# Kernel optimization log

Hardware: AMD Instinct MI355X
Metric: run time of the kernel (lower is better)

## Reference

```python
import jax, jax.numpy as jnp
import numpy as np

B, C, H = 256, 5, 13
N_AGENTS = 8192
N_EDGES = 262144
ACT = 21


def setup_inputs() -> dict:
    key = jax.random.key(0)
    ks = jax.random.split(key, 20)
    inp = {
        "x": jax.random.normal(ks[0], (B, C, H, H), jnp.float32),
        "x_msg": jax.random.normal(ks[1], (N_AGENTS,), jnp.float32),
        "edge_index": jax.random.randint(ks[2], (N_EDGES, 2), 0, N_AGENTS, jnp.int64 if jax.config.jax_enable_x64 else jnp.int32),
        "action": jax.random.randint(ks[3], (B,), 0, ACT, jnp.int32),
        # params (orthogonal init approximated by scaled normal; math identical)
        "conv1_w": jax.random.normal(ks[4], (32, 5, 3, 3), jnp.float32) * 0.1,
        "conv1_b": jnp.zeros((32,), jnp.float32),
        "conv2_w": jax.random.normal(ks[5], (64, 32, 3, 3), jnp.float32) * 0.05,
        "conv2_b": jnp.zeros((64,), jnp.float32),
        "fc_w": jax.random.normal(ks[6], (512, 1024), jnp.float32) * 0.03,
        "fc_b": jnp.zeros((512,), jnp.float32),
        "fc_mu_w": jax.random.normal(ks[7], (ACT, 512), jnp.float32) * 0.01,
        "fc_mu_b": jnp.zeros((ACT,), jnp.float32),
        "msg_w": jax.random.normal(ks[8], (N_AGENTS, 512), jnp.float32) * 0.01,
        "msg_b": jnp.zeros((N_AGENTS,), jnp.float32),
        "gcn1_w": jax.random.normal(ks[9], (2, 16), jnp.float32) * 0.5,
        "gcn1_b": jnp.zeros((16,), jnp.float32),
        "gcn2_w": jax.random.normal(ks[10], (16, N_AGENTS), jnp.float32) * 0.1,
        "gcn2_b": jnp.zeros((N_AGENTS,), jnp.float32),
    }
    return inp


def _gcn_norm(edge_index, n):
    # add self-loops; edge_index is (E,2) [src, dst]
    loops = jnp.arange(n, dtype=edge_index.dtype)
    src = jnp.concatenate([edge_index[:, 0], loops])
    dst = jnp.concatenate([edge_index[:, 1], loops])
    deg = jax.ops.segment_sum(jnp.ones_like(src, jnp.float32), dst, num_segments=n)
    dinv = jnp.where(deg > 0, jax.lax.rsqrt(deg), 0.0)
    norm = dinv[src] * dinv[dst]  # [E+n]
    return src, dst, norm


def _gcn_conv(h, src, dst, norm, W, b, n):
    hw = h @ W  # [n, out]
    out = jax.ops.segment_sum(norm[:, None] * hw[src], dst, num_segments=n)
    return out + b


def reference(x, x_msg, edge_index, action, conv1_w, conv1_b, conv2_w, conv2_b,
              fc_w, fc_b, fc_mu_w, fc_mu_b, msg_w, msg_b,
              gcn1_w, gcn1_b, gcn2_w, gcn2_b):
    dn = ("NCHW", "OIHW", "NCHW")
    h = jax.lax.conv_general_dilated(x, conv1_w, (2, 2), "VALID", dimension_numbers=dn)
    h = jax.nn.relu(h + conv1_b[None, :, None, None])  # [B,32,6,6]
    h = jax.lax.conv_general_dilated(h, conv2_w, (1, 1), "VALID", dimension_numbers=dn)
    h = jax.nn.relu(h + conv2_b[None, :, None, None])  # [B,64,4,4]
    h = h.reshape(h.shape[0], -1)  # [B,1024], torch NCHW flatten order
    hidden = jax.nn.relu(h @ fc_w.T + fc_b)  # [B,512]

    logits = hidden @ fc_mu_w.T + fc_mu_b            # [B,21]
    actor_encoding = hidden @ msg_w.T + msg_b        # [B,N]

    # Categorical log_prob / entropy for the given action
    logp = jax.nn.log_softmax(logits, axis=-1)
    log_prob = jnp.take_along_axis(logp, action[:, None], axis=1)[:, 0]
    entropy = -jnp.sum(jnp.exp(logp) * logp, axis=-1)

    # GNN message branch (eval mode: dropout is identity)
    feats = jnp.stack([x_msg, actor_encoding[0]], axis=0).T  # [N,2]
    n = feats.shape[0]
    src, dst, norm = _gcn_norm(edge_index, n)
    g = jax.nn.relu(_gcn_conv(feats, src, dst, norm, gcn1_w, gcn1_b, n))  # [N,16]
    g = _gcn_conv(g, src, dst, norm, gcn2_w, gcn2_b, n)                    # [N,N]
    msg_out = jax.nn.log_softmax(g, axis=1).mean(axis=1)                   # [N]

    return (action, msg_out, log_prob, entropy)
```

## Files before the change

kernel.cpp:

```cpp
#include <hip/hip_runtime.h>
#include <hip/hip_bf16.h>

#define NB 256
#define NACT 21
#define NA 8192
#define NE 262144
#define CSR_CAP 128
#define LOG2E 1.44269504f

#if __has_builtin(__builtin_amdgcn_exp2f)
#define EXP2F(x) __builtin_amdgcn_exp2f(x)
#else
#define EXP2F(x) exp2f(x)
#endif

typedef __attribute__((ext_vector_type(8))) short short8;
typedef __attribute__((ext_vector_type(4))) float float4v;

__device__ inline float wsum64(float v) {
#pragma unroll
  for (int m = 32; m > 0; m >>= 1) v += __shfl_xor(v, m, 64);
  return v;
}

__device__ inline unsigned short f2bf(float f) {
  union { __hip_bfloat16 h; unsigned short u; } cv;
  cv.h = __float2bfloat16(f);
  return cv.u;
}

__global__ void k_init(const int* action, int* cnt, float* out) {
  int i = blockIdx.x * 256 + threadIdx.x;
  if (i < NA) cnt[i] = 0;
  if (i < NB) out[i] = (float)action[i];
}

__global__ __launch_bounds__(512, 4) void k_prep(
    const int* __restrict__ edges, const float* __restrict__ fcw,
    const float* __restrict__ g2w, const float* __restrict__ g2b,
    unsigned short* fcwbf, unsigned short* w2t, float* wpart, int* cnt, int* csr) {
  __shared__ float red[16][17];
  __shared__ float b2s[16];
  int t = threadIdx.x, blk = blockIdx.x;
  {
    int e = blk * 512 + t;
    int s = edges[2 * e], d = edges[2 * e + 1];
    int slot = atomicAdd(&cnt[d], 1);
    if (slot < CSR_CAP) csr[d * CSR_CAP + slot] = s;
  }
  {
    int base = (blk * 512 + t) * 2;
    float2 v = *(const float2*)&fcw[base];
    fcwbf[base + 0] = f2bf(v.x);
    fcwbf[base + 1] = f2bf(v.y);
  }
  {
    if (t < 256) {
      int jj = t >> 4, k = t & 15;
      int j = blk * 16 + jj;
      float w = g2w[k * 8192 + j];
      w2t[j * 16 + k] = f2bf(w);
      red[jj][k] = w;
    }
    if (t < 16) b2s[t] = g2b[blk * 16 + t];
    __syncthreads();
    if (t < 16) {
      float s = 0.0f;
#pragma unroll
      for (int q = 0; q < 16; q++) s += red[q][t];
      wpart[blk * 17 + t] = s;
    } else if (t == 16) {
      float s = 0.0f;
#pragma unroll
      for (int q = 0; q < 16; q++) s += b2s[q];
      wpart[blk * 17 + 16] = s;
    }
  }
}

__global__ __launch_bounds__(512, 2) void k_conv(
    const float* __restrict__ x, const float* __restrict__ c1w, const float* __restrict__ c1b,
    const float* __restrict__ c2w, const float* __restrict__ c2b, unsigned short* h1024bf) {
  __shared__ float xs[845];
  __shared__ float w1s[1440];
  __shared__ float c1s[1152];
  __shared__ float w2s[64 * 73];
  int t = threadIdx.x, blk = blockIdx.x;
  for (int i = t; i < 845; i += 512) xs[i] = x[blk * 845 + i];
  for (int i = t; i < 1440; i += 512) w1s[i] = c1w[i];
  __syncthreads();
  for (int idx = t; idx < 1152; idx += 512) {
    int oc = idx / 36, p = idx - oc * 36;
    int oy = p / 6, ox = p - oy * 6;
    float acc = c1b[oc];
    const float* wp = &w1s[oc * 45];
#pragma unroll
    for (int ic = 0; ic < 5; ic++)
#pragma unroll
      for (int ky = 0; ky < 3; ky++)
#pragma unroll
        for (int kx = 0; kx < 3; kx++)
          acc += xs[ic * 169 + (oy * 2 + ky) * 13 + ox * 2 + kx] * wp[ic * 9 + ky * 3 + kx];
    c1s[idx] = fmaxf(acc, 0.0f);
  }
  int p = t & 15, oc2 = t >> 4;
  int oy = p >> 2, ox = p & 3;
  float a0 = c2b[oc2 * 2 + 0], a1 = c2b[oc2 * 2 + 1];
  for (int icb = 0; icb < 32; icb += 8) {
    __syncthreads();
    for (int i = t; i < 4608; i += 512) {
      int oc = i / 72, r = i - oc * 72;
      w2s[oc * 73 + r] = c2w[oc * 288 + icb * 9 + r];
    }
    __syncthreads();
#pragma unroll
    for (int ic = 0; ic < 8; ic++) {
#pragma unroll
      for (int ky = 0; ky < 3; ky++) {
#pragma unroll
        for (int kx = 0; kx < 3; kx++) {
          float cvv = c1s[(icb + ic) * 36 + (oy + ky) * 6 + ox + kx];
          int wi = ic * 9 + ky * 3 + kx;
          a0 += cvv * w2s[(oc2 * 2 + 0) * 73 + wi];
          a1 += cvv * w2s[(oc2 * 2 + 1) * 73 + wi];
        }
      }
    }
  }
  unsigned short* hp = &h1024bf[blk * 1024];
  hp[(oc2 * 2 + 0) * 16 + p] = f2bf(fmaxf(a0, 0.0f));
  hp[(oc2 * 2 + 1) * 16 + p] = f2bf(fmaxf(a1, 0.0f));
}

__global__ __launch_bounds__(256, 4) void k_fc(
    const int* __restrict__ cnt, const float* __restrict__ x_msg,
    const unsigned short* __restrict__ h1024bf, const unsigned short* __restrict__ fcwbf,
    const float* __restrict__ fcb, float* hidden, float* dinv, float* xs2) {
  __shared__ float red[4][256];
  int t = threadIdx.x, blk = blockIdx.x;
  int wave = t >> 6, lane = t & 63;
  if (blk < 32) {
    int i = blk * 256 + t;
    float d = rsqrtf((float)cnt[i] + 1.0f);
    dinv[i] = d;
    xs2[i] = d * x_msg[i];
  }
  int tr = blk >> 5, tc = blk & 31;
  int m = lane & 15, quad = lane >> 4;
  const unsigned short* ap = &h1024bf[(tr * 16 + m) * 1024 + wave * 256 + quad * 8];
  const unsigned short* bp = &fcwbf[(tc * 16 + m) * 1024 + wave * 256 + quad * 8];
  float4v acc = {0.0f, 0.0f, 0.0f, 0.0f};
#pragma unroll
  for (int i = 0; i < 8; i++) {
    short8 a = *(const short8*)(ap + i * 32);
    short8 b = *(const short8*)(bp + i * 32);
    acc = __builtin_amdgcn_mfma_f32_16x16x32_bf16(a, b, acc, 0, 0, 0);
  }
#pragma unroll
  for (int r = 0; r < 4; r++) red[wave][(quad * 4 + r) * 16 + m] = acc[r];
  __syncthreads();
  {
    float s = red[0][t] + red[1][t] + red[2][t] + red[3][t];
    int gr = tr * 16 + (t >> 4);
    int gc = tc * 16 + (t & 15);
    hidden[gr * 512 + gc] = fmaxf(s + fcb[gc], 0.0f);
  }
}

__global__ __launch_bounds__(512, 2) void k_he(
    const float* __restrict__ hidden, const float* __restrict__ muw,
    const float* __restrict__ mub, const float* __restrict__ msgw,
    const float* __restrict__ msgb, const float* __restrict__ dinv,
    float* es2, float* out) {
  __shared__ float muT[10752];
  __shared__ float hrows[2048];
  int t = threadIdx.x, blk = blockIdx.x;
  int wave = t >> 6, lane = t & 63;
  if (blk < 64) {
    int b0 = blk * 4;
    for (int i = t; i < 10752; i += 512) {
      int a = i >> 9, k = i & 511;
      muT[k * 21 + a] = muw[i];
    }
    for (int i = t; i < 2048; i += 512) hrows[i] = hidden[b0 * 512 + i];
    __syncthreads();
    if (wave < 4) {
      int b = b0 + wave;
      float logit = -1e30f;
      if (lane < NACT) {
        float acc = mub[lane];
        const float* hr = &hrows[wave * 512];
        for (int k = 0; k < 512; k++) acc += hr[k] * muT[k * 21 + lane];
        logit = acc;
      }
      float m = logit;
#pragma unroll
      for (int s = 32; s > 0; s >>= 1) m = fmaxf(m, __shfl_xor(m, s, 64));
      float e = (lane < NACT) ? __expf(logit - m) : 0.0f;
      float se = wsum64(e);
      float swl = wsum64(e * logit);
      float lse = m + __logf(se);
      if (lane == 0) out[8704 + b] = lse - swl / se;
      int act = (int)out[b];
      if (lane == act) out[8448 + b] = logit - lse;
    }
  } else {
    int wg = (blk - 64) * 8 + wave;
    for (int j = wg; j < NA; j += 3584) {
      const float* wp = &msgw[j * 512 + lane * 8];
      float4 w0 = *(const float4*)(wp);
      float4 w1 = *(const float4*)(wp + 4);
      float4 h0 = *(const float4*)&hidden[lane * 8];
      float4 h1 = *(const float4*)&hidden[lane * 8 + 4];
      float s = w0.x * h0.x + w0.y * h0.y + w0.z * h0.z + w0.w * h0.w +
                w1.x * h1.x + w1.y * h1.y + w1.z * h1.z + w1.w * h1.w;
      s = wsum64(s);
      if (lane == 0) es2[j] = dinv[j] * (s + msgb[j]);
    }
  }
}

__global__ __launch_bounds__(512, 4) void k_g1(
    const int* __restrict__ cnt, const int* __restrict__ csr,
    const float* __restrict__ dinv, const float* __restrict__ xs2,
    const float* __restrict__ es2, const float* __restrict__ g1w,
    const float* __restrict__ g1b, float* gbuf2) {
  int t = threadIdx.x, blk = blockIdx.x;
  int wave = t >> 6, lane = t & 63;
  int wg = blk * 8 + wave;
#pragma unroll
  for (int rr = 0; rr < 2; rr++) {
    int i = wg * 2 + rr;
    int ci = min(cnt[i], CSR_CAP);
    float di = dinv[i];
    float a0 = 0.0f, a1 = 0.0f;
    for (int e = lane; e < ci; e += 64) {
      int s = csr[i * CSR_CAP + e];
      a0 += xs2[s];
      a1 += es2[s];
    }
    float f0 = (wsum64(a0) + xs2[i]) * di;
    float f1 = (wsum64(a1) + es2[i]) * di;
    if (lane < 16) {
      float gv = fmaxf(f0 * g1w[lane] + f1 * g1w[16 + lane] + g1b[lane], 0.0f);
      gbuf2[i * 16 + lane] = di * gv;
    }
  }
}

__global__ __launch_bounds__(512, 2) void k_msg(
    const int* __restrict__ cnt, const int* __restrict__ csr,
    const float* __restrict__ dinv, const float* __restrict__ gbuf2,
    const float* __restrict__ wpart, const unsigned short* __restrict__ w2t,
    const float* __restrict__ g2b, float* out) {
  __shared__ __align__(16) unsigned short vbf[512];
  __shared__ float vf[512];
  __shared__ float pl[4096];
  __shared__ float sl[256];
  __shared__ float wp[16][17];
  __shared__ float wsf[17];
  int t = threadIdx.x, blk = blockIdx.x;
  int wave = t >> 6, lane = t & 63;
  int rowbase = blk * 32;
  {
    int eq = lane >> 4, c = lane & 15;
#pragma unroll
    for (int rr = 0; rr < 4; rr++) {
      int il = wave * 4 + rr;
      int i = rowbase + il;
      int ci = min(cnt[i], CSR_CAP);
      float di = dinv[i];
      float acc = (eq == 0) ? gbuf2[i * 16 + c] : 0.0f;
      for (int e = eq; e < ci; e += 4) {
        int s = csr[i * CSR_CAP + e];
        acc += gbuf2[s * 16 + c];
      }
      acc *= di;
      acc += __shfl_xor(acc, 16, 64);
      acc += __shfl_xor(acc, 32, 64);
      if (eq == 0) {
        vf[il * 16 + c] = acc;
        vbf[il * 16 + c] = f2bf(acc * LOG2E);
      }
    }
  }
  __syncthreads();
  if (t < 272) {
    int bq = t / 17, k = t - bq * 17;
    float s = 0.0f;
    for (int b = bq; b < 512; b += 16) s += wpart[b * 17 + k];
    wp[bq][k] = s;
  }
  __syncthreads();
  if (t < 17) {
    float s = 0.0f;
#pragma unroll
    for (int q = 0; q < 16; q++) s += wp[q][t];
    wsf[t] = s;
  }
  __syncthreads();
  float myMean = 0.0f;
  if (t < 32) {
    float dot = 0.0f;
#pragma unroll
    for (int c = 0; c < 16; c++) dot += vf[t * 16 + c] * wsf[c];
    myMean = (dot + wsf[16]) * (1.0f / 8192.0f);
  }
  {
    int quad = lane >> 4, n = lane & 15;
    int k8 = quad * 8;
    short8 za = {0, 0, 0, 0, 0, 0, 0, 0};
    short8 a1 = za, a2 = za;
    if (quad < 2) {
      a1 = *(const short8*)&vbf[n * 16 + k8];
      a2 = *(const short8*)&vbf[(16 + n) * 16 + k8];
    }
    float sacc[8];
#pragma unroll
    for (int q = 0; q < 8; q++) sacc[q] = 0.0f;
    int colb = wave * 1024 + n;
    for (int tp = 0; tp < 64; tp += 2) {
      int col1 = colb + tp * 16;
      int col2 = col1 + 16;
      short8 b1 = za, b2 = za;
      if (quad < 2) {
        b1 = *(const short8*)&w2t[col1 * 16 + k8];
        b2 = *(const short8*)&w2t[col2 * 16 + k8];
      }
      float bb1 = g2b[col1] * LOG2E, bb2 = g2b[col2] * LOG2E;
      float4v c1 = {bb1, bb1, bb1, bb1};
      float4v c2 = {bb2, bb2, bb2, bb2};
      float4v s11 = __builtin_amdgcn_mfma_f32_16x16x32_bf16(a1, b1, c1, 0, 0, 0);
      float4v s21 = __builtin_amdgcn_mfma_f32_16x16x32_bf16(a2, b1, c1, 0, 0, 0);
      float4v s12 = __builtin_amdgcn_mfma_f32_16x16x32_bf16(a1, b2, c2, 0, 0, 0);
      float4v s22 = __builtin_amdgcn_mfma_f32_16x16x32_bf16(a2, b2, c2, 0, 0, 0);
#pragma unroll
      for (int r = 0; r < 4; r++) {
        sacc[r]     += EXP2F(s11[r]) + EXP2F(s12[r]);
        sacc[4 + r] += EXP2F(s21[r]) + EXP2F(s22[r]);
      }
    }
#pragma unroll
    for (int q = 0; q < 8; q++) {
      int rl = (q >> 2) * 16 + quad * 4 + (q & 3);
      pl[rl * 128 + wave * 16 + n] = sacc[q];
    }
  }
  __syncthreads();
  if (t < 256) {
    int r = t >> 3, seg = t & 7;
    int base = r * 128 + seg * 16;
    float ll = 0.0f;
#pragma unroll
    for (int i = 0; i < 16; i++) ll += pl[base + i];
    sl[r * 8 + seg] = ll;
  }
  __syncthreads();
  if (t < 32) {
    float ll = 0.0f;
#pragma unroll
    for (int i = 0; i < 8; i++) ll += sl[t * 8 + i];
    out[256 + rowbase + t] = myMean - __logf(ll);
  }
}

extern "C" void kernel_launch(void* const* d_in, const int* in_sizes, int n_in,
                              void* d_out, int out_size, void* d_ws, size_t ws_size,
                              hipStream_t stream) {
  const float* x     = (const float*)d_in[0];
  const float* x_msg = (const float*)d_in[1];
  const int*   edges = (const int*)d_in[2];
  const int*   action= (const int*)d_in[3];
  const float* c1w   = (const float*)d_in[4];
  const float* c1b   = (const float*)d_in[5];
  const float* c2w   = (const float*)d_in[6];
  const float* c2b   = (const float*)d_in[7];
  const float* fcw   = (const float*)d_in[8];
  const float* fcb   = (const float*)d_in[9];
  const float* muw   = (const float*)d_in[10];
  const float* mub   = (const float*)d_in[11];
  const float* msgw  = (const float*)d_in[12];
  const float* msgb  = (const float*)d_in[13];
  const float* g1w   = (const float*)d_in[14];
  const float* g1b   = (const float*)d_in[15];
  const float* g2w   = (const float*)d_in[16];
  const float* g2b   = (const float*)d_in[17];
  float* out = (float*)d_out;

  float* ws     = (float*)d_ws;
  unsigned short* h1024bf = (unsigned short*)ws;
  unsigned short* fcwbf   = (unsigned short*)(ws + 131072);
  float* hidden = ws + 393216;
  float* es2    = ws + 524288;
  float* dinv   = ws + 532480;
  float* xs2    = ws + 540672;
  float* gbuf2  = ws + 548864;
  float* wpart  = ws + 679936;
  unsigned short* w2t = (unsigned short*)(ws + 688640);
  int*   cnt    = (int*)(ws + 754176);
  int*   csr    = (int*)(ws + 762368);

  k_init<<<33, 256, 0, stream>>>(action, cnt, out);
  k_prep<<<512, 512, 0, stream>>>(edges, fcw, g2w, g2b, fcwbf, w2t, wpart, cnt, csr);
  k_conv<<<256, 512, 0, stream>>>(x, c1w, c1b, c2w, c2b, h1024bf);
  k_fc  <<<512, 256, 0, stream>>>(cnt, x_msg, h1024bf, fcwbf, fcb, hidden, dinv, xs2);
  k_he  <<<512, 512, 0, stream>>>(hidden, muw, mub, msgw, msgb, dinv, es2, out);
  k_g1  <<<512, 512, 0, stream>>>(cnt, csr, dinv, xs2, es2, g1w, g1b, gbuf2);
  k_msg <<<256, 512, 0, stream>>>(cnt, csr, dinv, gbuf2, wpart, w2t, g2b, out);
}
```

Measured before the change: 188.6 us.

## Merge prep and conv kernels, hoist weight reduction, halve rows per msg block

Fuses the edge/weight prep kernel and the conv kernel into one launch, with block ranges selecting the role and a shared LDS pool. The per-block reduction of wpart in k_msg is moved into a single extra block of k_fc, so each k_msg block reads 17 precomputed sums instead of reducing 512 partials. k_msg now handles 16 rows per block with one MFMA A-operand, so it launches twice as many blocks. The action copy moves from k_init into k_he, removing one launch's worth of work. The trade-off is that each k_msg block re-reads the full w2t for half as many rows, which doubles w2t traffic in exchange for more parallelism.

After: 183.7 us. 1.03x faster.

```diff
diff --git a/kernel.cpp b/kernel.cpp
--- a/kernel.cpp
+++ b/kernel.cpp
@@ -29,115 +29,125 @@
   return cv.u;
 }
 
-__global__ void k_init(const int* action, int* cnt, float* out) {
-  int i = blockIdx.x * 256 + threadIdx.x;
-  if (i < NA) cnt[i] = 0;
-  if (i < NB) out[i] = (float)action[i];
-}
-
-__global__ __launch_bounds__(512, 4) void k_prep(
+__global__ __launch_bounds__(512) void k_init(int* cnt) {
+  int i = blockIdx.x * 512 + threadIdx.x;
+  cnt[i] = 0;
+}
+
+__global__ __launch_bounds__(512, 2) void k_pc(
     const int* __restrict__ edges, const float* __restrict__ fcw,
     const float* __restrict__ g2w, const float* __restrict__ g2b,
-    unsigned short* fcwbf, unsigned short* w2t, float* wpart, int* cnt, int* csr) {
-  __shared__ float red[16][17];
-  __shared__ float b2s[16];
-  int t = threadIdx.x, blk = blockIdx.x;
-  {
-    int e = blk * 512 + t;
-    int s = edges[2 * e], d = edges[2 * e + 1];
-    int slot = atomicAdd(&cnt[d], 1);
-    if (slot < CSR_CAP) csr[d * CSR_CAP + slot] = s;
-  }
-  {
-    int base = (blk * 512 + t) * 2;
-    float2 v = *(const float2*)&fcw[base];
-    fcwbf[base + 0] = f2bf(v.x);
-    fcwbf[base + 1] = f2bf(v.y);
-  }
-  {
-    if (t < 256) {
-      int jj = t >> 4, k = t & 15;
-      int j = blk * 16 + jj;
-      float w = g2w[k * 8192 + j];
-      w2t[j * 16 + k] = f2bf(w);
-      red[jj][k] = w;
-    }
-    if (t < 16) b2s[t] = g2b[blk * 16 + t];
-    __syncthreads();
-    if (t < 16) {
-      float s = 0.0f;
-#pragma unroll
-      for (int q = 0; q < 16; q++) s += red[q][t];
-      wpart[blk * 17 + t] = s;
-    } else if (t == 16) {
-      float s = 0.0f;
-#pragma unroll
-      for (int q = 0; q < 16; q++) s += b2s[q];
-      wpart[blk * 17 + 16] = s;
-    }
-  }
-}
-
-__global__ __launch_bounds__(512, 2) void k_conv(
+    unsigned short* fcwbf, unsigned short* w2t, float* wpart, int* cnt, int* csr,
     const float* __restrict__ x, const float* __restrict__ c1w, const float* __restrict__ c1b,
     const float* __restrict__ c2w, const float* __restrict__ c2b, unsigned short* h1024bf) {
-  __shared__ float xs[845];
-  __shared__ float w1s[1440];
-  __shared__ float c1s[1152];
-  __shared__ float w2s[64 * 73];
-  int t = threadIdx.x, blk = blockIdx.x;
-  for (int i = t; i < 845; i += 512) xs[i] = x[blk * 845 + i];
-  for (int i = t; i < 1440; i += 512) w1s[i] = c1w[i];
-  __syncthreads();
-  for (int idx = t; idx < 1152; idx += 512) {
-    int oc = idx / 36, p = idx - oc * 36;
-    int oy = p / 6, ox = p - oy * 6;
-    float acc = c1b[oc];
-    const float* wp = &w1s[oc * 45];
-#pragma unroll
-    for (int ic = 0; ic < 5; ic++)
-#pragma unroll
-      for (int ky = 0; ky < 3; ky++)
-#pragma unroll
-        for (int kx = 0; kx < 3; kx++)
-          acc += xs[ic * 169 + (oy * 2 + ky) * 13 + ox * 2 + kx] * wp[ic * 9 + ky * 3 + kx];
-    c1s[idx] = fmaxf(acc, 0.0f);
-  }
-  int p = t & 15, oc2 = t >> 4;
-  int oy = p >> 2, ox = p & 3;
-  float a0 = c2b[oc2 * 2 + 0], a1 = c2b[oc2 * 2 + 1];
-  for (int icb = 0; icb < 32; icb += 8) {
+  __shared__ float sm[8109];
+  int t = threadIdx.x;
+  if (blockIdx.x < 512) {
+    float (*red)[17] = (float(*)[17])sm;
+    float* b2s = sm + 272;
+    int blk = blockIdx.x;
+    {
+      int e = blk * 512 + t;
+      int s = edges[2 * e], d = edges[2 * e + 1];
+      int slot = atomicAdd(&cnt[d], 1);
+      if (slot < CSR_CAP) csr[d * CSR_CAP + slot] = s;
+    }
+    {
+      int base = (blk * 512 + t) * 2;
+      float2 v = *(const float2*)&fcw[base];
+      fcwbf[base + 0] = f2bf(v.x);
+      fcwbf[base + 1] = f2bf(v.y);
+    }
+    {
+      if (t < 256) {
+        int jj = t >> 4, k = t & 15;
+        int j = blk * 16 + jj;
+        float w = g2w[k * 8192 + j];
+        w2t[j * 16 + k] = f2bf(w);
+        red[jj][k] = w;
+      }
+      if (t < 16) b2s[t] = g2b[blk * 16 + t];
+      __syncthreads();
+      if (t < 16) {
+        float s = 0.0f;
+#pragma unroll
+        for (int q = 0; q < 16; q++) s += red[q][t];
+        wpart[blk * 17 + t] = s;
+      } else if (t == 16) {
+        float s = 0.0f;
+#pragma unroll
+        for (int q = 0; q < 16; q++) s += b2s[q];
+        wpart[blk * 17 + 16] = s;
+      }
+    }
+  } else {
+    float* xs = sm;
+    float* w1s = sm + 845;
+    float* c1s = sm + 2285;
+    float* w2s = sm + 3437;
+    int blk = blockIdx.x - 512;
+    for (int i = t; i < 845; i += 512) xs[i] = x[blk * 845 + i];
+    for (int i = t; i < 1440; i += 512) w1s[i] = c1w[i];
     __syncthreads();
-    for (int i = t; i < 4608; i += 512) {
-      int oc = i / 72, r = i - oc * 72;
-      w2s[oc * 73 + r] = c2w[oc * 288 + icb * 9 + r];
-    }
-    __syncthreads();
-#pragma unroll
-    for (int ic = 0; ic < 8; ic++) {
-#pragma unroll
-      for (int ky = 0; ky < 3; ky++) {
-#pragma unroll
-        for (int kx = 0; kx < 3; kx++) {
-          float cvv = c1s[(icb + ic) * 36 + (oy + ky) * 6 + ox + kx];
-          int wi = ic * 9 + ky * 3 + kx;
-          a0 += cvv * w2s[(oc2 * 2 + 0) * 73 + wi];
-          a1 += cvv * w2s[(oc2 * 2 + 1) * 73 + wi];
+    for (int idx = t; idx < 1152; idx += 512) {
+      int oc = idx / 36, p = idx - oc * 36;
+      int oy = p / 6, ox = p - oy * 6;
+      float acc = c1b[oc];
+      const float* wp = &w1s[oc * 45];
+#pragma unroll
+      for (int ic = 0; ic < 5; ic++)
+#pragma unroll
+        for (int ky = 0; ky < 3; ky++)
+#pragma unroll
+          for (int kx = 0; kx < 3; kx++)
+            acc += xs[ic * 169 + (oy * 2 + ky) * 13 + ox * 2 + kx] * wp[ic * 9 + ky * 3 + kx];
+      c1s[idx] = fmaxf(acc, 0.0f);
+    }
+    int p = t & 15, oc2 = t >> 4;
+    int oy = p >> 2, ox = p & 3;
+    float a0 = c2b[oc2 * 2 + 0], a1 = c2b[oc2 * 2 + 1];
+    for (int icb = 0; icb < 32; icb += 8) {
+      __syncthreads();
+      for (int i = t; i < 4608; i += 512) {
+        int oc = i / 72, r = i - oc * 72;
+        w2s[oc * 73 + r] = c2w[oc * 288 + icb * 9 + r];
+      }
+      __syncthreads();
+#pragma unroll
+      for (int ic = 0; ic < 8; ic++) {
+#pragma unroll
+        for (int ky = 0; ky < 3; ky++) {
+#pragma unroll
+          for (int kx = 0; kx < 3; kx++) {
+            float cvv = c1s[(icb + ic) * 36 + (oy + ky) * 6 + ox + kx];
+            int wi = ic * 9 + ky * 3 + kx;
+            a0 += cvv * w2s[(oc2 * 2 + 0) * 73 + wi];
+            a1 += cvv * w2s[(oc2 * 2 + 1) * 73 + wi];
+          }
         }
       }
     }
-  }
-  unsigned short* hp = &h1024bf[blk * 1024];
-  hp[(oc2 * 2 + 0) * 16 + p] = f2bf(fmaxf(a0, 0.0f));
-  hp[(oc2 * 2 + 1) * 16 + p] = f2bf(fmaxf(a1, 0.0f));
+    unsigned short* hp = &h1024bf[blk * 1024];
+    hp[(oc2 * 2 + 0) * 16 + p] = f2bf(fmaxf(a0, 0.0f));
+    hp[(oc2 * 2 + 1) * 16 + p] = f2bf(fmaxf(a1, 0.0f));
+  }
 }
 
 __global__ __launch_bounds__(256, 4) void k_fc(
     const int* __restrict__ cnt, const float* __restrict__ x_msg,
     const unsigned short* __restrict__ h1024bf, const unsigned short* __restrict__ fcwbf,
-    const float* __restrict__ fcb, float* hidden, float* dinv, float* xs2) {
+    const float* __restrict__ fcb, const float* __restrict__ wpart,
+    float* hidden, float* dinv, float* xs2, float* wsf) {
   __shared__ float red[4][256];
   int t = threadIdx.x, blk = blockIdx.x;
+  if (blk == 512) {
+    if (t < 17) {
+      float s = 0.0f;
+      for (int b = 0; b < 512; b++) s += wpart[b * 17 + t];
+      wsf[t] = s;
+    }
+    return;
+  }
   int wave = t >> 6, lane = t & 63;
   if (blk < 32) {
     int i = blk * 256 + t;
@@ -171,7 +181,7 @@
     const float* __restrict__ hidden, const float* __restrict__ muw,
     const float* __restrict__ mub, const float* __restrict__ msgw,
     const float* __restrict__ msgb, const float* __restrict__ dinv,
-    float* es2, float* out) {
+    const int* __restrict__ action, float* es2, float* out) {
   __shared__ float muT[10752];
   __shared__ float hrows[2048];
   int t = threadIdx.x, blk = blockIdx.x;
@@ -200,8 +210,11 @@
       float se = wsum64(e);
       float swl = wsum64(e * logit);
       float lse = m + __logf(se);
-      if (lane == 0) out[8704 + b] = lse - swl / se;
-      int act = (int)out[b];
+      int act = action[b];
+      if (lane == 0) {
+        out[b] = (float)act;
+        out[8704 + b] = lse - swl / se;
+      }
       if (lane == act) out[8448 + b] = logit - lse;
     }
   } else {
@@ -251,22 +264,22 @@
 __global__ __launch_bounds__(512, 2) void k_msg(
     const int* __restrict__ cnt, const int* __restrict__ csr,
     const float* __restrict__ dinv, const float* __restrict__ gbuf2,
-    const float* __restrict__ wpart, const unsigned short* __restrict__ w2t,
+    const float* __restrict__ wsf, const unsigned short* __restrict__ w2t,
     const float* __restrict__ g2b, float* out) {
-  __shared__ __align__(16) unsigned short vbf[512];
-  __shared__ float vf[512];
-  __shared__ float pl[4096];
-  __shared__ float sl[256];
-  __shared__ float wp[16][17];
-  __shared__ float wsf[17];
+  __shared__ __align__(16) unsigned short vbf[256];
+  __shared__ float vf[256];
+  __shared__ float pl[2048];
+  __shared__ float sl[128];
+  __shared__ float wsfs[17];
   int t = threadIdx.x, blk = blockIdx.x;
   int wave = t >> 6, lane = t & 63;
-  int rowbase = blk * 32;
+  int rowbase = blk * 16;
+  if (t < 17) wsfs[t] = wsf[t];
   {
     int eq = lane >> 4, c = lane & 15;
 #pragma unroll
-    for (int rr = 0; rr < 4; rr++) {
-      int il = wave * 4 + rr;
+    for (int rr = 0; rr < 2; rr++) {
+      int il = wave * 2 + rr;
       int i = rowbase + il;
       int ci = min(cnt[i], CSR_CAP);
       float di = dinv[i];
@@ -285,39 +298,22 @@
     }
   }
   __syncthreads();
-  if (t < 272) {
-    int bq = t / 17, k = t - bq * 17;
-    float s = 0.0f;
-    for (int b = bq; b < 512; b += 16) s += wpart[b * 17 + k];
-    wp[bq][k] = s;
-  }
-  __syncthreads();
-  if (t < 17) {
-    float s = 0.0f;
-#pragma unroll
-    for (int q = 0; q < 16; q++) s += wp[q][t];
-    wsf[t] = s;
-  }
-  __syncthreads();
   float myMean = 0.0f;
-  if (t < 32) {
+  if (t < 16) {
     float dot = 0.0f;
 #pragma unroll
-    for (int c = 0; c < 16; c++) dot += vf[t * 16 + c] * wsf[c];
-    myMean = (dot + wsf[16]) * (1.0f / 8192.0f);
+    for (int c = 0; c < 16; c++) dot += vf[t * 16 + c] * wsfs[c];
+    myMean = (dot + wsfs[16]) * (1.0f / 8192.0f);
   }
   {
     int quad = lane >> 4, n = lane & 15;
     int k8 = quad * 8;
     short8 za = {0, 0, 0, 0, 0, 0, 0, 0};
-    short8 a1 = za, a2 = za;
-    if (quad < 2) {
-      a1 = *(const short8*)&vbf[n * 16 + k8];
-      a2 = *(const short8*)&vbf[(16 + n) * 16 + k8];
-    }
-    float sacc[8];
-#pragma unroll
-    for (int q = 0; q < 8; q++) sacc[q] = 0.0f;
+    short8 a1 = za;
+    if (quad < 2) a1 = *(const short8*)&vbf[n * 16 + k8];
+    float sacc[4];
+#pragma unroll
+    for (int q = 0; q < 4; q++) sacc[q] = 0.0f;
     int colb = wave * 1024 + n;
     for (int tp = 0; tp < 64; tp += 2) {
       int col1 = colb + tp * 16;
@@ -331,23 +327,18 @@
       float4v c1 = {bb1, bb1, bb1, bb1};
       float4v c2 = {bb2, bb2, bb2, bb2};
       float4v s11 = __builtin_amdgcn_mfma_f32_16x16x32_bf16(a1, b1, c1, 0, 0, 0);
-      float4v s21 = __builtin_amdgcn_mfma_f32_16x16x32_bf16(a2, b1, c1, 0, 0, 0);
       float4v s12 = __builtin_amdgcn_mfma_f32_16x16x32_bf16(a1, b2, c2, 0, 0, 0);
-      float4v s22 = __builtin_amdgcn_mfma_f32_16x16x32_bf16(a2, b2, c2, 0, 0, 0);
-#pragma unroll
-      for (int r = 0; r < 4; r++) {
-        sacc[r]     += EXP2F(s11[r]) + EXP2F(s12[r]);
-        sacc[4 + r] += EXP2F(s21[r]) + EXP2F(s22[r]);
-      }
-    }
-#pragma unroll
-    for (int q = 0; q < 8; q++) {
-      int rl = (q >> 2) * 16 + quad * 4 + (q & 3);
+#pragma unroll
+      for (int r = 0; r < 4; r++) sacc[r] += EXP2F(s11[r]) + EXP2F(s12[r]);
+    }
+#pragma unroll
+    for (int q = 0; q < 4; q++) {
+      int rl = quad * 4 + q;
       pl[rl * 128 + wave * 16 + n] = sacc[q];
     }
   }
   __syncthreads();
-  if (t < 256) {
+  if (t < 128) {
     int r = t >> 3, seg = t & 7;
     int base = r * 128 + seg * 16;
     float ll = 0.0f;
@@ -356,7 +347,7 @@
     sl[r * 8 + seg] = ll;
   }
   __syncthreads();
-  if (t < 32) {
+  if (t < 16) {
     float ll = 0.0f;
 #pragma unroll
     for (int i = 0; i < 8; i++) ll += sl[t * 8 + i];
@@ -399,12 +390,13 @@
   unsigned short* w2t = (unsigned short*)(ws + 688640);
   int*   cnt    = (int*)(ws + 754176);
   int*   csr    = (int*)(ws + 762368);
-
-  k_init<<<33, 256, 0, stream>>>(action, cnt, out);
-  k_prep<<<512, 512, 0, stream>>>(edges, fcw, g2w, g2b, fcwbf, w2t, wpart, cnt, csr);
-  k_conv<<<256, 512, 0, stream>>>(x, c1w, c1b, c2w, c2b, h1024bf);
-  k_fc  <<<512, 256, 0, stream>>>(cnt, x_msg, h1024bf, fcwbf, fcb, hidden, dinv, xs2);
-  k_he  <<<512, 512, 0, stream>>>(hidden, muw, mub, msgw, msgb, dinv, es2, out);
-  k_g1  <<<512, 512, 0, stream>>>(cnt, csr, dinv, xs2, es2, g1w, g1b, gbuf2);
-  k_msg <<<256, 512, 0, stream>>>(cnt, csr, dinv, gbuf2, wpart, w2t, g2b, out);
-}
+  float* wsf    = ws + 1810944;
+
+  k_init<<<16, 512, 0, stream>>>(cnt);
+  k_pc <<<768, 512, 0, stream>>>(edges, fcw, g2w, g2b, fcwbf, w2t, wpart, cnt, csr,
+                                 x, c1w, c1b, c2w, c2b, h1024bf);
+  k_fc <<<513, 256, 0, stream>>>(cnt, x_msg, h1024bf, fcwbf, fcb, wpart, hidden, dinv, xs2, wsf);
+  k_he <<<512, 512, 0, stream>>>(hidden, muw, mub, msgw, msgb, dinv, action, es2, out);
+  k_g1 <<<512, 512, 0, stream>>>(cnt, csr, dinv, xs2, es2, g1w, g1b, gbuf2);
+  k_msg<<<512, 512, 0, stream>>>(cnt, csr, dinv, gbuf2, wsf, w2t, g2b, out);
+}
```
